# Performance work log

Hardware: AMD Instinct MI355X
Metric: run time of the kernel (lower is better)

## Reference

```python
import jax, jax.numpy as jnp
import numpy as np

H = 12  # n_heads

def setup_inputs() -> dict:
    key = jax.random.key(0)
    ks = jax.random.split(key, 7)
    dim = 768
    x = jax.random.normal(ks[0], (2, 8, 4, 256, dim), dtype=jnp.float32)
    s = dim ** -0.5
    Wq = jax.random.normal(ks[1], (dim, dim), dtype=jnp.float32) * s
    bq = jax.random.normal(ks[2], (dim,), dtype=jnp.float32) * 0.01
    Wk = jax.random.normal(ks[3], (dim, dim), dtype=jnp.float32) * s
    bk = jax.random.normal(ks[4], (dim,), dtype=jnp.float32) * 0.01
    Wv = jax.random.normal(ks[5], (dim, dim), dtype=jnp.float32) * s
    bv = jax.random.normal(ks[6], (dim,), dtype=jnp.float32) * 0.01
    return {"x": x, "Wq": Wq, "bq": bq, "Wk": Wk, "bk": bk, "Wv": Wv, "bv": bv}

def _split_heads(y):
    # [b,t,l,p,(h d)] -> [b,t,l,h,p,d]
    b, t, l, p, hd = y.shape
    return y.reshape(b, t, l, p, H, hd // H).transpose(0, 1, 2, 4, 3, 5)

def reference(x, Wq, bq, Wk, bk, Wv, bv):
    dim = x.shape[-1]
    scale = (dim / H) ** -0.5
    q = _split_heads(x @ Wq.T + bq)  # [b,t,l,h,p,d]
    k = _split_heads(x @ Wk.T + bk)
    v = _split_heads(x @ Wv.T + bv)
    dots = jnp.einsum('btlhpd,btlhqd->btlhpq', q, k) * scale
    attn = jax.nn.softmax(dots, axis=-1)
    out = jnp.einsum('btlhpq,btlhqd->btlhpd', attn, v)
    # [b,t,l,h,p,d] -> [b,t,l,p,(h d)]
    b, t, l, h, p, d = out.shape
    return out.transpose(0, 1, 2, 4, 3, 5).reshape(b, t, l, p, h * d)
```

## Files before the change

### kernel.cpp

```cpp
#include <hip/hip_runtime.h>

typedef _Float16 f16;
typedef __attribute__((ext_vector_type(2))) _Float16 f16x2;
typedef __attribute__((ext_vector_type(8))) _Float16 f16x8;
typedef __attribute__((ext_vector_type(4))) float f32x4;

#define MFMA16(a,b,c) __builtin_amdgcn_mfma_f32_16x16x32_f16(a,b,c,0,0,0)

constexpr int NSEQ = 64;
constexpr int P    = 256;
constexpr int DIMF = 768;
constexpr int NH   = 12;
constexpr int DH   = 64;
constexpr int M    = NSEQ * P;
constexpr size_t XSZ = (size_t)M * DIMF;
constexpr size_t WSZ = (size_t)DIMF * DIMF;

__device__ __forceinline__ f16x8 cvt8(const float* p) {
    const float4 u = *(const float4*)p;
    const float4 w = *(const float4*)(p + 4);
    f16x2 a = __builtin_bit_cast(f16x2, __builtin_amdgcn_cvt_pkrtz(u.x, u.y));
    f16x2 b = __builtin_bit_cast(f16x2, __builtin_amdgcn_cvt_pkrtz(u.z, u.w));
    f16x2 c = __builtin_bit_cast(f16x2, __builtin_amdgcn_cvt_pkrtz(w.x, w.y));
    f16x2 d = __builtin_bit_cast(f16x2, __builtin_amdgcn_cvt_pkrtz(w.z, w.w));
    f16x8 r;
    r[0]=a[0]; r[1]=a[1]; r[2]=b[0]; r[3]=b[1];
    r[4]=c[0]; r[5]=c[1]; r[6]=d[0]; r[7]=d[1];
    return r;
}

__device__ __forceinline__ void gload16(const void* g, void* l) {
    __builtin_amdgcn_global_load_lds(
        (const __attribute__((address_space(1))) void*)g,
        (__attribute__((address_space(3))) void*)l, 16, 0, 0);
}

__global__ __launch_bounds__(256) void conv_kernel(
    const float* __restrict__ x,
    const float* __restrict__ Wq, const float* __restrict__ Wk,
    const float* __restrict__ Wv,
    f16* __restrict__ xh, f16* __restrict__ wh)
{
    const size_t i8 = ((size_t)blockIdx.x * 256 + threadIdx.x) * 8;
    if (i8 < XSZ) {
        *(f16x8*)(xh + i8) = cvt8(x + i8);
    } else {
        const size_t j = i8 - XSZ;
        const int mtx = (int)(j / WSZ);
        const size_t r = j - (size_t)mtx * WSZ;
        const float* src = (mtx == 0 ? Wq : mtx == 1 ? Wk : Wv) + r;
        *(f16x8*)(wh + j) = cvt8(src);
    }
}

__global__ __launch_bounds__(512, 2) void proj_gemm(
    const f16* __restrict__ xh, const f16* __restrict__ wh,
    const float* __restrict__ bq, const float* __restrict__ bk,
    const float* __restrict__ bv,
    f16* __restrict__ qout, f16* __restrict__ kout, f16* __restrict__ vt)
{
    __shared__ __align__(16) char smem[131072];
    const int wg = (blockIdx.x & 7) * 72 + (blockIdx.x >> 3);
    const int nt = wg % 9;
    const int mt = wg / 9;
    const int m0 = mt * 256, n0 = nt * 256;

    const int tid  = threadIdx.x;
    const int lane = tid & 63;
    const int wave = tid >> 6;
    const int lr   = lane & 15;
    const int lg   = lane >> 4;
    const int wm   = wave >> 2;
    const int wn   = wave & 3;

    const int srow = tid >> 3, scc = tid & 7;
    const f16* gA = xh + (size_t)(m0 + srow) * DIMF + (scc ^ (srow & 7)) * 8;
    const f16* gB = wh + (size_t)(n0 + srow) * DIMF + (scc ^ (srow & 7)) * 8;

    const int swz0 = (lg ^ (lr & 7)) * 16;
    const char* pA0 = smem + (wm * 128 + lr) * 128;
    const char* pB0 = smem + 65536 + (wn * 64 + lr) * 128;

    f32x4 acc[8][4];
    #pragma unroll
    for (int f = 0; f < 8; ++f)
        #pragma unroll
        for (int g = 0; g < 4; ++g) acc[f][g] = (f32x4){0.f,0.f,0.f,0.f};

    #pragma unroll
    for (int q = 0; q < 4; ++q) {
        gload16(gA + (size_t)q * (64*DIMF), smem + q*8192 + tid*16);
        gload16(gB + (size_t)q * (64*DIMF), smem + 65536 + q*8192 + tid*16);
    }

    f16x8 a[4][2], bf[2][2];

    #pragma unroll 2
    for (int kt = 0; kt < 12; ++kt) {
        const int b = kt & 1;
        const char* lA = pA0 + b * 32768;
        const char* lB = pB0 + b * 32768;
        char* sA = smem + (b ^ 1) * 32768;
        char* sB = sA + 65536;
        const f16* ga = gA + (kt + 1) * 64;
        const f16* gb = gB + (kt + 1) * 64;
        const bool st = kt < 11;

        __builtin_amdgcn_s_barrier();

        if (st) { gload16(ga, sA + tid*16); gload16(gb, sB + tid*16); }
        if (st) asm volatile("s_waitcnt vmcnt(2)" ::: "memory");
        else    asm volatile("s_waitcnt vmcnt(0)" ::: "memory");
        __builtin_amdgcn_s_barrier();
        __builtin_amdgcn_sched_barrier(0);
        #pragma unroll
        for (int f = 0; f < 4; ++f) {
            a[f][0] = *(const f16x8*)(lA + f*2048 + swz0);
            a[f][1] = *(const f16x8*)(lA + f*2048 + (swz0 ^ 64));
        }
        #pragma unroll
        for (int f = 0; f < 2; ++f) {
            bf[f][0] = *(const f16x8*)(lB + f*2048 + swz0);
            bf[f][1] = *(const f16x8*)(lB + f*2048 + (swz0 ^ 64));
        }
        __builtin_amdgcn_s_setprio(1);
        #pragma unroll
        for (int f = 0; f < 4; ++f)
            #pragma unroll
            for (int g = 0; g < 2; ++g) {
                acc[f][g] = MFMA16(a[f][0], bf[g][0], acc[f][g]);
                acc[f][g] = MFMA16(a[f][1], bf[g][1], acc[f][g]);
            }
        __builtin_amdgcn_s_setprio(0);

        if (st) { gload16(ga + (size_t)(64*DIMF), sA + 8192 + tid*16);
                  gload16(gb + (size_t)(64*DIMF), sB + 8192 + tid*16); }
        #pragma unroll
        for (int f = 0; f < 2; ++f) {
            bf[f][0] = *(const f16x8*)(lB + (2+f)*2048 + swz0);
            bf[f][1] = *(const f16x8*)(lB + (2+f)*2048 + (swz0 ^ 64));
        }
        __builtin_amdgcn_s_barrier();
        __builtin_amdgcn_s_setprio(1);
        #pragma unroll
        for (int f = 0; f < 4; ++f)
            #pragma unroll
            for (int g = 0; g < 2; ++g) {
                acc[f][2+g] = MFMA16(a[f][0], bf[g][0], acc[f][2+g]);
                acc[f][2+g] = MFMA16(a[f][1], bf[g][1], acc[f][2+g]);
            }
        __builtin_amdgcn_s_setprio(0);

        if (st) { gload16(ga + (size_t)(128*DIMF), sA + 16384 + tid*16);
                  gload16(gb + (size_t)(128*DIMF), sB + 16384 + tid*16); }
        #pragma unroll
        for (int f = 0; f < 4; ++f) {
            a[f][0] = *(const f16x8*)(lA + (4+f)*2048 + swz0);
            a[f][1] = *(const f16x8*)(lA + (4+f)*2048 + (swz0 ^ 64));
        }
        __builtin_amdgcn_s_barrier();
        __builtin_amdgcn_s_setprio(1);
        #pragma unroll
        for (int f = 0; f < 4; ++f)
            #pragma unroll
            for (int g = 0; g < 2; ++g) {
                acc[4+f][2+g] = MFMA16(a[f][0], bf[g][0], acc[4+f][2+g]);
                acc[4+f][2+g] = MFMA16(a[f][1], bf[g][1], acc[4+f][2+g]);
            }
        __builtin_amdgcn_s_setprio(0);

        if (st) { gload16(ga + (size_t)(192*DIMF), sA + 24576 + tid*16);
                  gload16(gb + (size_t)(192*DIMF), sB + 24576 + tid*16); }
        #pragma unroll
        for (int f = 0; f < 2; ++f) {
            bf[f][0] = *(const f16x8*)(lB + f*2048 + swz0);
            bf[f][1] = *(const f16x8*)(lB + f*2048 + (swz0 ^ 64));
        }
        __builtin_amdgcn_s_barrier();
        __builtin_amdgcn_s_setprio(1);
        #pragma unroll
        for (int f = 0; f < 4; ++f)
            #pragma unroll
            for (int g = 0; g < 2; ++g) {
                acc[4+f][g] = MFMA16(a[f][0], bf[g][0], acc[4+f][g]);
                acc[4+f][g] = MFMA16(a[f][1], bf[g][1], acc[4+f][g]);
            }
        __builtin_amdgcn_s_setprio(0);
    }

    __syncthreads();

    const int mat = nt / 3;
    const int c0  = (nt % 3) * 256;
    const int seq = mt;
    const float* __restrict__ bias = mat == 0 ? bq : mat == 1 ? bk : bv;
    float bb[4];
    #pragma unroll
    for (int g = 0; g < 4; ++g) bb[g] = bias[c0 + wn*64 + g*16 + lr];

    f16 (*ep)[264] = (f16 (*)[264])smem;
    #pragma unroll
    for (int hh = 0; hh < 2; ++hh) {
        if (wm == hh) {
            #pragma unroll
            for (int f = 0; f < 8; ++f)
                #pragma unroll
                for (int g = 0; g < 4; ++g)
                    #pragma unroll
                    for (int i = 0; i < 4; ++i)
                        ep[f*16 + lg*4 + i][wn*64 + g*16 + lr] =
                            (f16)(acc[f][g][i] + bb[g]);
        }
        __syncthreads();
        if (mat < 2) {
            f16* __restrict__ dst = mat ? kout : qout;
            const int r = tid >> 2;
            #pragma unroll
            for (int s = 0; s < 8; ++s) {
                const int ch = s*4 + (tid & 3);
                const int h  = (nt % 3) * 4 + (ch >> 3);
                const int d0 = (ch & 7) * 8;
                *(f16x8*)(dst + ((size_t)(seq*NH + h)*P + hh*128 + r)*DH + d0) =
                    *(const f16x8*)&ep[r][ch*8];
            }
        } else {
            const int col = tid >> 1, rg = tid & 1;
            const int h = (nt % 3) * 4 + (col >> 6), d = col & 63;
            f16* drow = vt + ((size_t)(seq*NH + h)*DH + d)*P + hh*128 + rg*64;
            #pragma unroll
            for (int u = 0; u < 8; ++u) {
                f16x8 vv;
                #pragma unroll
                for (int uu = 0; uu < 8; ++uu)
                    vv[uu] = ep[rg*64 + u*8 + uu][col];
                *(f16x8*)(drow + u*8) = vv;
            }
        }
        __syncthreads();
    }
}

__global__ __launch_bounds__(512) void attn_kernel(
    const f16* __restrict__ q, const f16* __restrict__ k,
    const f16* __restrict__ vt, float* __restrict__ out)
{
    __shared__ __align__(16) char kl[32768];
    __shared__ __align__(16) char vl[32768];
    __shared__ __align__(16) char pl[8][2048];

    const int n = blockIdx.x;
    const int b = (n & 7) * 192 + (n >> 3);
    const int half = b & 1;
    const int head = (b >> 1) % NH;
    const int seq  = b / (2 * NH);

    const int tid  = threadIdx.x;
    const int lane = tid & 63;
    const int wave = tid >> 6;
    const int lr   = lane & 15;
    const int lg   = lane >> 4;

    const f16* qh = q  + (size_t)(seq*NH + head)*P*DH;
    const f16* kh = k  + (size_t)(seq*NH + head)*P*DH;
    const f16* vh = vt + (size_t)(seq*NH + head)*DH*P;

    {
        const int r0 = tid >> 3, ck = tid & 7;
        const int d0 = tid >> 5, cv = tid & 31;
        #pragma unroll
        for (int it = 0; it < 4; ++it) {
            const int row = it * 64 + r0;
            gload16(kh + row * 64 + ((ck ^ (row & 7)) * 8), kl + it * 8192 + tid * 16);
            const int d = it * 16 + d0;
            gload16(vh + d * 256 + (((cv & 24) | ((cv ^ d) & 7)) * 8), vl + it * 8192 + tid * 16);
        }
    }

    const int qr0 = half * 128 + wave * 16;
    const f16x8 aq0 = *(const f16x8*)(qh + (qr0 + lr) * DH + lg * 8);
    const f16x8 aq1 = *(const f16x8*)(qh + (qr0 + lr) * DH + 32 + lg * 8);

    __syncthreads();

    f32x4 s[16];
    #pragma unroll
    for (int t = 0; t < 16; ++t) s[t] = (f32x4){0.f,0.f,0.f,0.f};
    #pragma unroll
    for (int t = 0; t < 16; ++t) {
        const int row = t * 16 + lr;
        const f16x8 b0 = *(const f16x8*)(kl + row * 128 + ((lg ^ (row & 7)) * 16));
        const f16x8 b1 = *(const f16x8*)(kl + row * 128 + (((lg + 4) ^ (row & 7)) * 16));
        s[t] = MFMA16(aq0, b0, s[t]);
        s[t] = MFMA16(aq1, b1, s[t]);
    }

    float mx[4] = {-1e30f, -1e30f, -1e30f, -1e30f};
    #pragma unroll
    for (int t = 0; t < 16; ++t)
        #pragma unroll
        for (int i = 0; i < 4; ++i) mx[i] = fmaxf(mx[i], s[t][i]);
    #pragma unroll
    for (int st = 1; st < 16; st <<= 1)
        #pragma unroll
        for (int i = 0; i < 4; ++i) mx[i] = fmaxf(mx[i], __shfl_xor(mx[i], st));

    const float SCL = 0.125f * 1.44269504088896f;
    float rs[4] = {0.f, 0.f, 0.f, 0.f};
    #pragma unroll
    for (int t = 0; t < 16; ++t)
        #pragma unroll
        for (int i = 0; i < 4; ++i) {
            const float e = exp2f((s[t][i] - mx[i]) * SCL);
            s[t][i] = e;
            rs[i] += e;
        }
    #pragma unroll
    for (int st = 1; st < 16; st <<= 1)
        #pragma unroll
        for (int i = 0; i < 4; ++i) rs[i] += __shfl_xor(rs[i], st);

    char* pw = pl[wave];
    f32x4 o[4];
    #pragma unroll
    for (int t = 0; t < 4; ++t) o[t] = (f32x4){0.f,0.f,0.f,0.f};

    #pragma unroll
    for (int qq = 0; qq < 4; ++qq) {
        #pragma unroll
        for (int tt = 0; tt < 4; ++tt) {
            const int t = qq * 4 + tt;
            #pragma unroll
            for (int i = 0; i < 4; ++i) {
                const int r = lg * 4 + i;
                const int klocal = tt * 16 + lr;
                *(f16*)(pw + r * 128 + ((klocal * 2) ^ ((r & 7) << 4))) = (f16)s[t][i];
            }
        }
        #pragma unroll
        for (int kol = 0; kol < 2; ++kol) {
            const f16x8 ap = *(const f16x8*)(pw + lr * 128 + (((kol * 4 + lg) ^ (lr & 7)) * 16));
            #pragma unroll
            for (int dt = 0; dt < 4; ++dt) {
                const int row = dt * 16 + lr;
                const int ch  = qq * 8 + kol * 4 + lg;
                const f16x8 bv_ = *(const f16x8*)(vl + row * 512 + (((ch & 24) | ((ch ^ row) & 7)) * 16));
                o[dt] = MFMA16(ap, bv_, o[dt]);
            }
        }
    }

    #pragma unroll
    for (int i = 0; i < 4; ++i) rs[i] = 1.f / rs[i];
    float* op = out + ((size_t)seq * P + qr0) * DIMF + head * DH;
    #pragma unroll
    for (int t = 0; t < 4; ++t)
        #pragma unroll
        for (int i = 0; i < 4; ++i)
            op[(lg * 4 + i) * DIMF + t * 16 + lr] = o[t][i] * rs[i];
}

extern "C" void kernel_launch(void* const* d_in, const int* in_sizes, int n_in,
                              void* d_out, int out_size, void* d_ws, size_t ws_size,
                              hipStream_t stream) {
    const float* x  = (const float*)d_in[0];
    const float* Wq = (const float*)d_in[1];
    const float* bq = (const float*)d_in[2];
    const float* Wk = (const float*)d_in[3];
    const float* bk = (const float*)d_in[4];
    const float* Wv = (const float*)d_in[5];
    const float* bv = (const float*)d_in[6];
    float* out = (float*)d_out;

    f16* xh = (f16*)d_out;
    f16* wh = xh + XSZ;

    const size_t QSZ = (size_t)M * DIMF;
    f16* q  = (f16*)d_ws;
    f16* k  = q + QSZ;
    f16* vt = k + QSZ;

    const int convThreads = (int)((XSZ + 3 * WSZ) / 8);
    conv_kernel<<<convThreads / 256, 256, 0, stream>>>(x, Wq, Wk, Wv, xh, wh);
    proj_gemm<<<dim3(576), 512, 0, stream>>>(xh, wh, bq, bk, bv, q, k, vt);
    attn_kernel<<<dim3(NSEQ * NH * 2), 512, 0, stream>>>(q, k, vt, out);
}
```

Measured before the change: 122.7 us.

## Make projection GEMM persistent with reordered loads and explicit LDS waits

The projection GEMM becomes a persistent kernel: 256 workgroups loop over the 576 tiles instead of launching one workgroup per tile, with launch bounds lowered to one block per CU. The global-to-LDS load order is reshuffled so B chunks arrive earlier and A chunks are split across phases, vmcnt waits are relaxed, and explicit lgkmcnt waits plus sched barriers are added before each MFMA group. The goal is to cut launch and tail effects and better overlap memory with MFMA. The cost is an uneven tile split (576 over 256 workgroups gives 2 or 3 tiles each), and the pipeline's correctness now depends on the new vmcnt counts.

```diff
diff --git a/kernel.cpp b/kernel.cpp
--- a/kernel.cpp
+++ b/kernel.cpp
@@ -53,18 +53,13 @@
     }
 }
 
-__global__ __launch_bounds__(512, 2) void proj_gemm(
+__global__ __launch_bounds__(512, 1) void proj_gemm(
     const f16* __restrict__ xh, const f16* __restrict__ wh,
     const float* __restrict__ bq, const float* __restrict__ bk,
     const float* __restrict__ bv,
     f16* __restrict__ qout, f16* __restrict__ kout, f16* __restrict__ vt)
 {
     __shared__ __align__(16) char smem[131072];
-    const int wg = (blockIdx.x & 7) * 72 + (blockIdx.x >> 3);
-    const int nt = wg % 9;
-    const int mt = wg / 9;
-    const int m0 = mt * 256, n0 = nt * 256;
-
     const int tid  = threadIdx.x;
     const int lane = tid & 63;
     const int wave = tid >> 6;
@@ -73,171 +68,199 @@
     const int wm   = wave >> 2;
     const int wn   = wave & 3;
 
-    const int srow = tid >> 3, scc = tid & 7;
-    const f16* gA = xh + (size_t)(m0 + srow) * DIMF + (scc ^ (srow & 7)) * 8;
-    const f16* gB = wh + (size_t)(n0 + srow) * DIMF + (scc ^ (srow & 7)) * 8;
-
     const int swz0 = (lg ^ (lr & 7)) * 16;
     const char* pA0 = smem + (wm * 128 + lr) * 128;
     const char* pB0 = smem + 65536 + (wn * 64 + lr) * 128;
 
-    f32x4 acc[8][4];
-    #pragma unroll
-    for (int f = 0; f < 8; ++f)
-        #pragma unroll
-        for (int g = 0; g < 4; ++g) acc[f][g] = (f32x4){0.f,0.f,0.f,0.f};
-
-    #pragma unroll
-    for (int q = 0; q < 4; ++q) {
-        gload16(gA + (size_t)q * (64*DIMF), smem + q*8192 + tid*16);
-        gload16(gB + (size_t)q * (64*DIMF), smem + 65536 + q*8192 + tid*16);
+    const int bid = (blockIdx.x & 7) * 32 + (blockIdx.x >> 3);
+
+    #define BAR  __builtin_amdgcn_s_barrier()
+    #define LGKM asm volatile("s_waitcnt lgkmcnt(0)" ::: "memory")
+    #define SCHB __builtin_amdgcn_sched_barrier(0)
+
+    for (int wg = bid; wg < 576; wg += 256) {
+        const int nt = wg % 9;
+        const int mt = wg / 9;
+        const int m0 = mt * 256, n0 = nt * 256;
+
+        const int srow = tid >> 3, scc = tid & 7;
+        const f16* gA = xh + (size_t)(m0 + srow) * DIMF + (scc ^ (srow & 7)) * 8;
+        const f16* gB = wh + (size_t)(n0 + srow) * DIMF + (scc ^ (srow & 7)) * 8;
+
+        f32x4 acc[8][4];
+        #pragma unroll
+        for (int f = 0; f < 8; ++f)
+            #pragma unroll
+            for (int g = 0; g < 4; ++g) acc[f][g] = (f32x4){0.f,0.f,0.f,0.f};
+
+        gload16(gA,                        smem + 0*8192  + tid*16);
+        gload16(gB,                        smem + 65536 + 0*8192 + tid*16);
+        gload16(gB + (size_t)( 64*DIMF),   smem + 65536 + 1*8192 + tid*16);
+        gload16(gB + (size_t)(128*DIMF),   smem + 65536 + 2*8192 + tid*16);
+        gload16(gB + (size_t)(192*DIMF),   smem + 65536 + 3*8192 + tid*16);
+        gload16(gA + (size_t)(128*DIMF),   smem + 2*8192  + tid*16);
+        SCHB;
+        gload16(gA + (size_t)( 64*DIMF),   smem + 1*8192  + tid*16);
+        gload16(gA + (size_t)(192*DIMF),   smem + 3*8192  + tid*16);
+
+        f16x8 a[4][2], bf[2][2];
+
+        for (int kt = 0; kt < 12; ++kt) {
+            const int b = kt & 1;
+            const char* lA = pA0 + b * 32768;
+            const char* lB = pB0 + b * 32768;
+            char* sA = smem + (b ^ 1) * 32768;
+            char* sB = sA + 65536;
+            const f16* ga = gA + (kt + 1) * 64;
+            const f16* gb = gB + (kt + 1) * 64;
+            const bool st = kt < 11;
+
+            BAR;
+
+            if (st) { gload16(ga, sA + tid*16); gload16(gb, sB + tid*16); }
+            SCHB;
+            if (st) asm volatile("s_waitcnt vmcnt(4)" ::: "memory");
+            else    asm volatile("s_waitcnt vmcnt(2)" ::: "memory");
+            BAR;
+            SCHB;
+            #pragma unroll
+            for (int f = 0; f < 4; ++f) {
+                a[f][0] = *(const f16x8*)(lA + f*2048 + swz0);
+                a[f][1] = *(const f16x8*)(lA + f*2048 + (swz0 ^ 64));
+            }
+            #pragma unroll
+            for (int f = 0; f < 2; ++f) {
+                bf[f][0] = *(const f16x8*)(lB + f*2048 + swz0);
+                bf[f][1] = *(const f16x8*)(lB + f*2048 + (swz0 ^ 64));
+            }
+            LGKM; SCHB;
+            __builtin_amdgcn_s_setprio(1);
+            #pragma unroll
+            for (int f = 0; f < 4; ++f)
+                #pragma unroll
+                for (int g = 0; g < 2; ++g) {
+                    acc[f][g] = MFMA16(a[f][0], bf[g][0], acc[f][g]);
+                    acc[f][g] = MFMA16(a[f][1], bf[g][1], acc[f][g]);
+                }
+            __builtin_amdgcn_s_setprio(0);
+
+            if (st) gload16(gb + (size_t)(64*DIMF), sB + 8192 + tid*16);
+            #pragma unroll
+            for (int f = 0; f < 2; ++f) {
+                bf[f][0] = *(const f16x8*)(lB + (2+f)*2048 + swz0);
+                bf[f][1] = *(const f16x8*)(lB + (2+f)*2048 + (swz0 ^ 64));
+            }
+            LGKM; SCHB;
+            __builtin_amdgcn_s_setprio(1);
+            #pragma unroll
+            for (int f = 0; f < 4; ++f)
+                #pragma unroll
+                for (int g = 0; g < 2; ++g) {
+                    acc[f][2+g] = MFMA16(a[f][0], bf[g][0], acc[f][2+g]);
+                    acc[f][2+g] = MFMA16(a[f][1], bf[g][1], acc[f][2+g]);
+                }
+            __builtin_amdgcn_s_setprio(0);
+
+            if (st) gload16(ga + (size_t)(128*DIMF), sA + 16384 + tid*16);
+            SCHB;
+            if (st) asm volatile("s_waitcnt vmcnt(4)" ::: "memory");
+            else    asm volatile("s_waitcnt vmcnt(0)" ::: "memory");
+            BAR;
+            SCHB;
+            #pragma unroll
+            for (int f = 0; f < 4; ++f) {
+                a[f][0] = *(const f16x8*)(lA + (4+f)*2048 + swz0);
+                a[f][1] = *(const f16x8*)(lA + (4+f)*2048 + (swz0 ^ 64));
+            }
+            LGKM; SCHB;
+            __builtin_amdgcn_s_setprio(1);
+            #pragma unroll
+            for (int f = 0; f < 4; ++f)
+                #pragma unroll
+                for (int g = 0; g < 2; ++g) {
+                    acc[4+f][2+g] = MFMA16(a[f][0], bf[g][0], acc[4+f][2+g]);
+                    acc[4+f][2+g] = MFMA16(a[f][1], bf[g][1], acc[4+f][2+g]);
+                }
+            __builtin_amdgcn_s_setprio(0);
+
+            if (st) {
+                gload16(gb + (size_t)(128*DIMF), sB + 16384 + tid*16);
+                gload16(gb + (size_t)(192*DIMF), sB + 24576 + tid*16);
+                SCHB;
+                gload16(ga + (size_t)( 64*DIMF), sA + 8192  + tid*16);
+                gload16(ga + (size_t)(192*DIMF), sA + 24576 + tid*16);
+            }
+            #pragma unroll
+            for (int f = 0; f < 2; ++f) {
+                bf[f][0] = *(const f16x8*)(lB + f*2048 + swz0);
+                bf[f][1] = *(const f16x8*)(lB + f*2048 + (swz0 ^ 64));
+            }
+            LGKM; SCHB;
+            __builtin_amdgcn_s_setprio(1);
+            #pragma unroll
+            for (int f = 0; f < 4; ++f)
+                #pragma unroll
+                for (int g = 0; g < 2; ++g) {
+                    acc[4+f][g] = MFMA16(a[f][0], bf[g][0], acc[4+f][g]);
+                    acc[4+f][g] = MFMA16(a[f][1], bf[g][1], acc[4+f][g]);
+                }
+            __builtin_amdgcn_s_setprio(0);
+        }
+
+        __syncthreads();
+
+        const int mat = nt / 3;
+        const int c0  = (nt % 3) * 256;
+        const int seq = mt;
+        const float* __restrict__ bias = mat == 0 ? bq : mat == 1 ? bk : bv;
+        float bb[4];
+        #pragma unroll
+        for (int g = 0; g < 4; ++g) bb[g] = bias[c0 + wn*64 + g*16 + lr];
+
+        f16 (*ep)[264] = (f16 (*)[264])smem;
+        #pragma unroll
+        for (int hh = 0; hh < 2; ++hh) {
+            if (wm == hh) {
+                #pragma unroll
+                for (int f = 0; f < 8; ++f)
+                    #pragma unroll
+                    for (int g = 0; g < 4; ++g)
+                        #pragma unroll
+                        for (int i = 0; i < 4; ++i)
+                            ep[f*16 + lg*4 + i][wn*64 + g*16 + lr] =
+                                (f16)(acc[f][g][i] + bb[g]);
+            }
+            __syncthreads();
+            if (mat < 2) {
+                f16* __restrict__ dst = mat ? kout : qout;
+                const int r = tid >> 2;
+                #pragma unroll
+                for (int s = 0; s < 8; ++s) {
+                    const int ch = s*4 + (tid & 3);
+                    const int h  = (nt % 3) * 4 + (ch >> 3);
+                    const int d0 = (ch & 7) * 8;
+                    *(f16x8*)(dst + ((size_t)(seq*NH + h)*P + hh*128 + r)*DH + d0) =
+                        *(const f16x8*)&ep[r][ch*8];
+                }
+            } else {
+                const int col = tid >> 1, rg = tid & 1;
+                const int h = (nt % 3) * 4 + (col >> 6), d = col & 63;
+                f16* drow = vt + ((size_t)(seq*NH + h)*DH + d)*P + hh*128 + rg*64;
+                #pragma unroll
+                for (int u = 0; u < 8; ++u) {
+                    f16x8 vv;
+                    #pragma unroll
+                    for (int uu = 0; uu < 8; ++uu)
+                        vv[uu] = ep[rg*64 + u*8 + uu][col];
+                    *(f16x8*)(drow + u*8) = vv;
+                }
+            }
+            __syncthreads();
+        }
     }
-
-    f16x8 a[4][2], bf[2][2];
-
-    #pragma unroll 2
-    for (int kt = 0; kt < 12; ++kt) {
-        const int b = kt & 1;
-        const char* lA = pA0 + b * 32768;
-        const char* lB = pB0 + b * 32768;
-        char* sA = smem + (b ^ 1) * 32768;
-        char* sB = sA + 65536;
-        const f16* ga = gA + (kt + 1) * 64;
-        const f16* gb = gB + (kt + 1) * 64;
-        const bool st = kt < 11;
-
-        __builtin_amdgcn_s_barrier();
-
-        if (st) { gload16(ga, sA + tid*16); gload16(gb, sB + tid*16); }
-        if (st) asm volatile("s_waitcnt vmcnt(2)" ::: "memory");
-        else    asm volatile("s_waitcnt vmcnt(0)" ::: "memory");
-        __builtin_amdgcn_s_barrier();
-        __builtin_amdgcn_sched_barrier(0);
-        #pragma unroll
-        for (int f = 0; f < 4; ++f) {
-            a[f][0] = *(const f16x8*)(lA + f*2048 + swz0);
-            a[f][1] = *(const f16x8*)(lA + f*2048 + (swz0 ^ 64));
-        }
-        #pragma unroll
-        for (int f = 0; f < 2; ++f) {
-            bf[f][0] = *(const f16x8*)(lB + f*2048 + swz0);
-            bf[f][1] = *(const f16x8*)(lB + f*2048 + (swz0 ^ 64));
-        }
-        __builtin_amdgcn_s_setprio(1);
-        #pragma unroll
-        for (int f = 0; f < 4; ++f)
-            #pragma unroll
-            for (int g = 0; g < 2; ++g) {
-                acc[f][g] = MFMA16(a[f][0], bf[g][0], acc[f][g]);
-                acc[f][g] = MFMA16(a[f][1], bf[g][1], acc[f][g]);
-            }
-        __builtin_amdgcn_s_setprio(0);
-
-        if (st) { gload16(ga + (size_t)(64*DIMF), sA + 8192 + tid*16);
-                  gload16(gb + (size_t)(64*DIMF), sB + 8192 + tid*16); }
-        #pragma unroll
-        for (int f = 0; f < 2; ++f) {
-            bf[f][0] = *(const f16x8*)(lB + (2+f)*2048 + swz0);
-            bf[f][1] = *(const f16x8*)(lB + (2+f)*2048 + (swz0 ^ 64));
-        }
-        __builtin_amdgcn_s_barrier();
-        __builtin_amdgcn_s_setprio(1);
-        #pragma unroll
-        for (int f = 0; f < 4; ++f)
-            #pragma unroll
-            for (int g = 0; g < 2; ++g) {
-                acc[f][2+g] = MFMA16(a[f][0], bf[g][0], acc[f][2+g]);
-                acc[f][2+g] = MFMA16(a[f][1], bf[g][1], acc[f][2+g]);
-            }
-        __builtin_amdgcn_s_setprio(0);
-
-        if (st) { gload16(ga + (size_t)(128*DIMF), sA + 16384 + tid*16);
-                  gload16(gb + (size_t)(128*DIMF), sB + 16384 + tid*16); }
-        #pragma unroll
-        for (int f = 0; f < 4; ++f) {
-            a[f][0] = *(const f16x8*)(lA + (4+f)*2048 + swz0);
-            a[f][1] = *(const f16x8*)(lA + (4+f)*2048 + (swz0 ^ 64));
-        }
-        __builtin_amdgcn_s_barrier();
-        __builtin_amdgcn_s_setprio(1);
-        #pragma unroll
-        for (int f = 0; f < 4; ++f)
-            #pragma unroll
-            for (int g = 0; g < 2; ++g) {
-                acc[4+f][2+g] = MFMA16(a[f][0], bf[g][0], acc[4+f][2+g]);
-                acc[4+f][2+g] = MFMA16(a[f][1], bf[g][1], acc[4+f][2+g]);
-            }
-        __builtin_amdgcn_s_setprio(0);
-
-        if (st) { gload16(ga + (size_t)(192*DIMF), sA + 24576 + tid*16);
-                  gload16(gb + (size_t)(192*DIMF), sB + 24576 + tid*16); }
-        #pragma unroll
-        for (int f = 0; f < 2; ++f) {
-            bf[f][0] = *(const f16x8*)(lB + f*2048 + swz0);
-            bf[f][1] = *(const f16x8*)(lB + f*2048 + (swz0 ^ 64));
-        }
-        __builtin_amdgcn_s_barrier();
-        __builtin_amdgcn_s_setprio(1);
-        #pragma unroll
-        for (int f = 0; f < 4; ++f)
-            #pragma unroll
-            for (int g = 0; g < 2; ++g) {
-                acc[4+f][g] = MFMA16(a[f][0], bf[g][0], acc[4+f][g]);
-                acc[4+f][g] = MFMA16(a[f][1], bf[g][1], acc[4+f][g]);
-            }
-        __builtin_amdgcn_s_setprio(0);
-    }
-
-    __syncthreads();
-
-    const int mat = nt / 3;
-    const int c0  = (nt % 3) * 256;
-    const int seq = mt;
-    const float* __restrict__ bias = mat == 0 ? bq : mat == 1 ? bk : bv;
-    float bb[4];
-    #pragma unroll
-    for (int g = 0; g < 4; ++g) bb[g] = bias[c0 + wn*64 + g*16 + lr];
-
-    f16 (*ep)[264] = (f16 (*)[264])smem;
-    #pragma unroll
-    for (int hh = 0; hh < 2; ++hh) {
-        if (wm == hh) {
-            #pragma unroll
-            for (int f = 0; f < 8; ++f)
-                #pragma unroll
-                for (int g = 0; g < 4; ++g)
-                    #pragma unroll
-                    for (int i = 0; i < 4; ++i)
-                        ep[f*16 + lg*4 + i][wn*64 + g*16 + lr] =
-                            (f16)(acc[f][g][i] + bb[g]);
-        }
-        __syncthreads();
-        if (mat < 2) {
-            f16* __restrict__ dst = mat ? kout : qout;
-            const int r = tid >> 2;
-            #pragma unroll
-            for (int s = 0; s < 8; ++s) {
-                const int ch = s*4 + (tid & 3);
-                const int h  = (nt % 3) * 4 + (ch >> 3);
-                const int d0 = (ch & 7) * 8;
-                *(f16x8*)(dst + ((size_t)(seq*NH + h)*P + hh*128 + r)*DH + d0) =
-                    *(const f16x8*)&ep[r][ch*8];
-            }
-        } else {
-            const int col = tid >> 1, rg = tid & 1;
-            const int h = (nt % 3) * 4 + (col >> 6), d = col & 63;
-            f16* drow = vt + ((size_t)(seq*NH + h)*DH + d)*P + hh*128 + rg*64;
-            #pragma unroll
-            for (int u = 0; u < 8; ++u) {
-                f16x8 vv;
-                #pragma unroll
-                for (int uu = 0; uu < 8; ++uu)
-                    vv[uu] = ep[rg*64 + u*8 + uu][col];
-                *(f16x8*)(drow + u*8) = vv;
-            }
-        }
-        __syncthreads();
-    }
+    #undef BAR
+    #undef LGKM
+    #undef SCHB
 }
 
 __global__ __launch_bounds__(512) void attn_kernel(
@@ -381,6 +404,6 @@
 
     const int convThreads = (int)((XSZ + 3 * WSZ) / 8);
     conv_kernel<<<convThreads / 256, 256, 0, stream>>>(x, Wq, Wk, Wv, xh, wh);
-    proj_gemm<<<dim3(576), 512, 0, stream>>>(xh, wh, bq, bk, bv, q, k, vt);
+    proj_gemm<<<dim3(256), 512, 0, stream>>>(xh, wh, bq, bk, bv, q, k, vt);
     attn_kernel<<<dim3(NSEQ * NH * 2), 512, 0, stream>>>(q, k, vt, out);
 }
```

Result: slower. 129.7 us (+5.7%).
